# Kernel optimization log

Hardware: AMD Instinct MI355X
Metric: run time of the kernel (lower is better)

The kernel has to match this reference:

```python
import jax, jax.numpy as jnp
import numpy as np

TOP_K = 10
RANKING_WEIGHT = 0.3
UP_WEIGHT = 1.0
DOWN_WEIGHT = 0.5
NEG = 1e9  # finite stand-in for -inf so softmax/grads stay NaN-free


def setup_inputs() -> dict:
    key = jax.random.key(0)
    k1, k2, k3, k4 = jax.random.split(key, 4)
    B, N = 1024, 5000
    up_logits = jax.random.normal(k1, (B, N), jnp.float32)
    down_logits = jax.random.normal(k2, (B, N), jnp.float32)
    y_true = jax.random.normal(k3, (B, N), jnp.float32) * 0.05  # daily returns
    masks = jax.random.randint(k4, (B, N), 0, 2).astype(jnp.int32)
    return {"up_logits": up_logits, "down_logits": down_logits,
            "y_true": y_true, "masks": masks}


def _bce_with_logits(x, z):
    # softplus(x) - x*z  ==  -[z*log(sig(x)) + (1-z)*log(1-sig(x))]
    return jax.nn.softplus(x) - x * z


def reference(up_logits, down_logits, y_true, masks):
    maskb = masks > 0                                   # [B, N]
    maskf = maskb.astype(up_logits.dtype)
    num_valid = maskf.sum(-1)                           # [B]
    nv_safe = jnp.maximum(num_valid, 1.0)
    k = jnp.minimum(TOP_K, num_valid.astype(jnp.int32))  # [B] min(top_k, num)

    # Descending rank of y_true among valid entries (invalid pushed to bottom).
    y_desc = jnp.where(maskb, y_true, -NEG)
    rank_desc = jnp.argsort(jnp.argsort(-y_desc, axis=-1), axis=-1)  # [B, N]
    up_labels = (rank_desc < k[:, None]).astype(up_logits.dtype)

    # Ascending rank (biggest losers) for down path.
    y_asc = jnp.where(maskb, y_true, NEG)
    rank_asc = jnp.argsort(jnp.argsort(y_asc, axis=-1), axis=-1)
    down_labels = (rank_asc < k[:, None]).astype(down_logits.dtype)

    # Mean BCE over valid entries per row.
    up_loss = jnp.sum(_bce_with_logits(up_logits, up_labels) * maskf, -1) / nv_safe
    down_loss = jnp.sum(_bce_with_logits(down_logits, down_labels) * maskf, -1) / nv_safe

    # Listwise KL: softmax over valid entries; kl_div(log p, q, 'batchmean')
    # with 1D input of size num divides the sum by num.
    logp = jax.nn.log_softmax(jnp.where(maskb, up_logits, -NEG), axis=-1)
    logq = jax.nn.log_softmax(jnp.where(maskb, y_true, -NEG), axis=-1)
    q = jnp.exp(logq)
    kl = jnp.sum(jnp.where(maskb, q * (logq - logp), 0.0), -1) / nv_safe

    batch_loss = UP_WEIGHT * up_loss + DOWN_WEIGHT * down_loss + RANKING_WEIGHT * kl
    batch_loss = jnp.where(num_valid > 0, batch_loss, 0.0)  # skip empty rows
    return jnp.sum(batch_loss) / up_logits.shape[0]
```

## Files before the change

### kernel.cpp

```cpp
#include <hip/hip_runtime.h>
#include <math.h>

#define NCOLS 5000
#define NF4   1250
#define BLOCK 256
#define NWAVES (BLOCK / 64)
#define NITER 5
#define TOPKK 10
#define CAP 384

__device__ __forceinline__ unsigned mono_f32(float f) {
  unsigned u = __float_as_uint(f);
  return (u & 0x80000000u) ? ~u : (u | 0x80000000u);
}

__device__ __forceinline__ float wave_sum_f(float v) {
#pragma unroll
  for (int o = 1; o < 64; o <<= 1) v += __shfl_xor(v, o);
  return v;
}
__device__ __forceinline__ int wave_sum_i(int v) {
#pragma unroll
  for (int o = 1; o < 64; o <<= 1) v += __shfl_xor(v, o);
  return v;
}
__device__ __forceinline__ unsigned wave_max_u(unsigned v) {
#pragma unroll
  for (int o = 1; o < 64; o <<= 1) {
    unsigned w = __shfl_xor(v, o);
    v = w > v ? w : v;
  }
  return v;
}

extern "C" __global__ __launch_bounds__(BLOCK, 4)
void row_loss_kernel(const float* __restrict__ up, const float* __restrict__ down,
                     const float* __restrict__ yt, const int* __restrict__ masks,
                     float* __restrict__ out, float inv_nrows) {
  __shared__ float red_f[6][NWAVES];
  __shared__ int red_i[NWAVES];
  __shared__ unsigned t1w_t[NWAVES];
  __shared__ unsigned t1w_b[NWAVES];
  __shared__ unsigned keys_t[CAP];
  __shared__ int      col_t[CAP];
  __shared__ unsigned keys_b[CAP];
  __shared__ int      col_b[CAP];
  __shared__ int ct, cb;
  __shared__ float s_res[2];

  const int tid = threadIdx.x;
  const int lane = tid & 63;
  const int wv = tid >> 6;
  const int row = blockIdx.x;
  const long long b4 = (long long)row * NF4;
  const long long base = (long long)row * NCOLS;

  const float4* up4 = (const float4*)up + b4;
  const float4* dn4 = (const float4*)down + b4;
  const float4* yt4 = (const float4*)yt + b4;
  const int4*   mk4 = (const int4*)masks + b4;

  if (tid == 0) { ct = 0; cb = 0; }

  unsigned km[NITER][4];
  int nv_l = 0;
  float sq = 0.f, sp = 0.f, seyy = 0.f, seyu = 0.f;
  float pu0 = 1.f, pu1 = 1.f, pd0 = 1.f, pd1 = 1.f;
  unsigned tmax = 0u, tbmax = 0u;
#pragma unroll
  for (int j = 0; j < NITER; ++j) {
    const int f = j * BLOCK + tid;
    const int fc = f < NF4 ? f : NF4 - 1;
    const float4 y4 = yt4[fc];
    const float4 u4 = up4[fc];
    const float4 d4 = dn4[fc];
    const int4   m4 = mk4[fc];
    const bool inb = f < NF4;
    const float* yp = (const float*)&y4;
    const float* upp = (const float*)&u4;
    const float* dp = (const float*)&d4;
    const int* mp = (const int*)&m4;
#pragma unroll
    for (int c = 0; c < 4; ++c) {
      const bool valid = inb && (mp[c] > 0);
      const float y = valid ? yp[c] : -1000.f;
      const float u = valid ? upp[c] : -1000.f;
      const float d = valid ? dp[c] : -1000.f;
      const unsigned kd = valid ? mono_f32(y) : 0u;
      const unsigned kb = valid ? ~kd : 0u;
      km[j][c] = kd;
      tmax = kd > tmax ? kd : tmax;
      tbmax = kb > tbmax ? kb : tbmax;
      nv_l += valid ? 1 : 0;
      const float ey = __expf(y);
      const float eu = __expf(u);
      const float ed = __expf(d);
      sq += ey;
      seyy += ey * y;
      seyu += ey * u;
      sp += eu;
      if (j < 3) { pu0 *= 1.f + eu; pd0 *= 1.f + ed; }
      else       { pu1 *= 1.f + eu; pd1 *= 1.f + ed; }
    }
  }
  float aspu = __logf(pu0) + __logf(pu1);
  float aspd = __logf(pd0) + __logf(pd1);

  nv_l = wave_sum_i(nv_l);
  sq = wave_sum_f(sq);
  sp = wave_sum_f(sp);
  seyy = wave_sum_f(seyy);
  seyu = wave_sum_f(seyu);
  aspu = wave_sum_f(aspu);
  aspd = wave_sum_f(aspd);
  if (lane == 0) {
    red_i[wv] = nv_l;
    red_f[0][wv] = sq;  red_f[1][wv] = sp;
    red_f[2][wv] = seyy; red_f[3][wv] = seyu;
    red_f[4][wv] = aspu; red_f[5][wv] = aspd;
  }

  {
    unsigned v = tmax, t1 = 0u;
#pragma unroll 1
    for (int r = 0; r < TOPKK; ++r) {
      unsigned m = wave_max_u(v);
      if (v == m) v = 0u;
      t1 = m;
    }
    if (lane == 0) t1w_t[wv] = t1;
  }
  {
    unsigned v = tbmax, t1 = 0u;
#pragma unroll 1
    for (int r = 0; r < TOPKK; ++r) {
      unsigned m = wave_max_u(v);
      if (v == m) v = 0u;
      t1 = m;
    }
    if (lane == 0) t1w_b[wv] = t1;
  }
  __syncthreads();

  int nv = 0;
#pragma unroll
  for (int w = 0; w < NWAVES; ++w) nv += red_i[w];
  const int k = nv < TOPKK ? nv : TOPKK;

  unsigned t1 = 0u, t1b = 0u;
#pragma unroll
  for (int w = 0; w < NWAVES; ++w) {
    t1 = t1w_t[w] > t1 ? t1w_t[w] : t1;
    t1b = t1w_b[w] > t1b ? t1w_b[w] : t1b;
  }

#pragma unroll
  for (int j = 0; j < NITER; ++j) {
#pragma unroll
    for (int c = 0; c < 4; ++c) {
      const unsigned kd = km[j][c];
      if (kd != 0u) {
        const int col = ((j * BLOCK + tid) << 2) + c;
        if (kd >= t1) {
          int i = atomicAdd(&ct, 1);
          if (i < CAP) { keys_t[i] = kd; col_t[i] = col; }
        }
        const unsigned kb = ~kd;
        if (kb >= t1b) {
          int i = atomicAdd(&cb, 1);
          if (i < CAP) { keys_b[i] = kb; col_b[i] = col; }
        }
      }
    }
  }
  __syncthreads();

  if (wv == 0) {
    const int n = ct < CAP ? ct : CAP;
    unsigned kk[6];
#pragma unroll
    for (int i = 0; i < 6; ++i) {
      const int idx = i * 64 + lane;
      kk[i] = (idx < n) ? keys_t[idx] : 0u;
    }
    unsigned w0 = kk[0], w1 = kk[1], w2 = kk[2], w3 = kk[3], w4 = kk[4], w5 = kk[5];
    unsigned thr = 0xFFFFFFFFu;
#pragma unroll 1
    for (int r = 0; r < k; ++r) {
      unsigned l0 = w0 > w1 ? w0 : w1;
      unsigned l1 = w2 > w3 ? w2 : w3;
      unsigned l2 = w4 > w5 ? w4 : w5;
      l0 = l0 > l1 ? l0 : l1;
      unsigned m = wave_max_u(l0 > l2 ? l0 : l2);
      if (w0 == m) w0 = 0u;
      else if (w1 == m) w1 = 0u;
      else if (w2 == m) w2 = 0u;
      else if (w3 == m) w3 = 0u;
      else if (w4 == m) w4 = 0u;
      else if (w5 == m) w5 = 0u;
      thr = m;
    }
    float su = 0.f;
#pragma unroll
    for (int i = 0; i < 6; ++i) {
      const int idx = i * 64 + lane;
      if (kk[i] >= thr && kk[i] != 0u) su += up[base + col_t[idx]];
    }
    su = wave_sum_f(su);
    if (lane == 0) s_res[0] = su;
  } else if (wv == 1) {
    const int n = cb < CAP ? cb : CAP;
    unsigned kk[6];
#pragma unroll
    for (int i = 0; i < 6; ++i) {
      const int idx = i * 64 + lane;
      kk[i] = (idx < n) ? keys_b[idx] : 0u;
    }
    unsigned w0 = kk[0], w1 = kk[1], w2 = kk[2], w3 = kk[3], w4 = kk[4], w5 = kk[5];
    unsigned thr = 0xFFFFFFFFu;
#pragma unroll 1
    for (int r = 0; r < k; ++r) {
      unsigned l0 = w0 > w1 ? w0 : w1;
      unsigned l1 = w2 > w3 ? w2 : w3;
      unsigned l2 = w4 > w5 ? w4 : w5;
      l0 = l0 > l1 ? l0 : l1;
      unsigned m = wave_max_u(l0 > l2 ? l0 : l2);
      if (w0 == m) w0 = 0u;
      else if (w1 == m) w1 = 0u;
      else if (w2 == m) w2 = 0u;
      else if (w3 == m) w3 = 0u;
      else if (w4 == m) w4 = 0u;
      else if (w5 == m) w5 = 0u;
      thr = m;
    }
    float sd = 0.f;
#pragma unroll
    for (int i = 0; i < 6; ++i) {
      const int idx = i * 64 + lane;
      if (kk[i] >= thr && kk[i] != 0u) sd += down[base + col_b[idx]];
    }
    sd = wave_sum_f(sd);
    if (lane == 0) s_res[1] = sd;
  }
  __syncthreads();

  if (tid == 0 && nv > 0) {
    float SQ = 0.f, SP = 0.f, SYY = 0.f, SYU = 0.f, ASU = 0.f, ASD = 0.f;
#pragma unroll
    for (int w = 0; w < NWAVES; ++w) {
      SQ += red_f[0][w]; SP += red_f[1][w];
      SYY += red_f[2][w]; SYU += red_f[3][w];
      ASU += red_f[4][w]; ASD += red_f[5][w];
    }
    const float SU = s_res[0];
    const float SD = s_res[1];
    const float kl = (SYY - SYU) / SQ - __logf(SQ) + __logf(SP);
    const float up_loss = ASU - SU;
    const float dn_loss = ASD - SD;
    const float loss = (up_loss + 0.5f * dn_loss + 0.3f * kl) / (float)nv;
    atomicAdd(out, loss * inv_nrows);
  }
}

extern "C" void kernel_launch(void* const* d_in, const int* in_sizes, int n_in,
                              void* d_out, int out_size, void* d_ws, size_t ws_size,
                              hipStream_t stream) {
  const float* up_logits   = (const float*)d_in[0];
  const float* down_logits = (const float*)d_in[1];
  const float* y_true      = (const float*)d_in[2];
  const int*   masks       = (const int*)d_in[3];

  const int nrows = in_sizes[0] / NCOLS;

  hipMemsetAsync(d_out, 0, sizeof(float) * (size_t)out_size, stream);
  row_loss_kernel<<<nrows, BLOCK, 0, stream>>>(up_logits, down_logits, y_true,
                                               masks, (float*)d_out,
                                               1.0f / (float)nrows);
}
```

Measured before the change: 125.0 us.

## Split each row across two blocks and merge per-half top-k in finalize kernel

Each row is now processed by two 640-thread blocks, each handling half the columns with a single float4 per thread. Each block writes partial sums plus its local top-10 keys and values to workspace. A second kernel merges the two halves per row and reduces the loss. Candidate values are stored in shared memory directly, so the later global gathers of logits go away. The aim is more parallelism and latency hiding, at the cost of an extra kernel launch and a workspace round trip.

```diff
diff --git a/kernel.cpp b/kernel.cpp
--- a/kernel.cpp
+++ b/kernel.cpp
@@ -3,11 +3,13 @@
 
 #define NCOLS 5000
 #define NF4   1250
-#define BLOCK 256
-#define NWAVES (BLOCK / 64)
-#define NITER 5
+#define HALF_F4 625
+#define BLOCK_A 640
+#define NWAVES_A 10
 #define TOPKK 10
-#define CAP 384
+#define CAP 512
+#define WS_STRIDE 48
+#define BLOCK_B 256
 
 __device__ __forceinline__ unsigned mono_f32(float f) {
   unsigned u = __float_as_uint(f);
@@ -33,78 +35,71 @@
   return v;
 }
 
-extern "C" __global__ __launch_bounds__(BLOCK, 4)
-void row_loss_kernel(const float* __restrict__ up, const float* __restrict__ down,
-                     const float* __restrict__ yt, const int* __restrict__ masks,
-                     float* __restrict__ out, float inv_nrows) {
-  __shared__ float red_f[6][NWAVES];
-  __shared__ int red_i[NWAVES];
-  __shared__ unsigned t1w_t[NWAVES];
-  __shared__ unsigned t1w_b[NWAVES];
-  __shared__ unsigned keys_t[CAP];
-  __shared__ int      col_t[CAP];
-  __shared__ unsigned keys_b[CAP];
-  __shared__ int      col_b[CAP];
+extern "C" __global__ __launch_bounds__(BLOCK_A)
+void partial_kernel(const float* __restrict__ up, const float* __restrict__ down,
+                    const float* __restrict__ yt, const int* __restrict__ masks,
+                    float* __restrict__ ws) {
+  __shared__ float red_f[6][NWAVES_A];
+  __shared__ int red_i[NWAVES_A];
+  __shared__ unsigned t1w_t[NWAVES_A], t1w_b[NWAVES_A];
+  __shared__ unsigned skeys_t[CAP];
+  __shared__ float    svals_t[CAP];
+  __shared__ unsigned skeys_b[CAP];
+  __shared__ float    svals_b[CAP];
   __shared__ int ct, cb;
-  __shared__ float s_res[2];
 
   const int tid = threadIdx.x;
   const int lane = tid & 63;
   const int wv = tid >> 6;
-  const int row = blockIdx.x;
-  const long long b4 = (long long)row * NF4;
-  const long long base = (long long)row * NCOLS;
-
-  const float4* up4 = (const float4*)up + b4;
-  const float4* dn4 = (const float4*)down + b4;
-  const float4* yt4 = (const float4*)yt + b4;
-  const int4*   mk4 = (const int4*)masks + b4;
+  const int half = blockIdx.x & 1;
+  const int row = blockIdx.x >> 1;
+  const long long b4 = (long long)row * NF4 + half * HALF_F4;
 
   if (tid == 0) { ct = 0; cb = 0; }
 
-  unsigned km[NITER][4];
+  const bool inb = tid < HALF_F4;
+  const int fo = inb ? tid : HALF_F4 - 1;
+  const float4 y4 = ((const float4*)yt)[b4 + fo];
+  const float4 u4 = ((const float4*)up)[b4 + fo];
+  const float4 d4 = ((const float4*)down)[b4 + fo];
+  const int4   m4 = ((const int4*)masks)[b4 + fo];
+
+  unsigned km[4];
+  float uv[4], dv[4];
   int nv_l = 0;
   float sq = 0.f, sp = 0.f, seyy = 0.f, seyu = 0.f;
-  float pu0 = 1.f, pu1 = 1.f, pd0 = 1.f, pd1 = 1.f;
+  float pu = 1.f, pd = 1.f;
   unsigned tmax = 0u, tbmax = 0u;
-#pragma unroll
-  for (int j = 0; j < NITER; ++j) {
-    const int f = j * BLOCK + tid;
-    const int fc = f < NF4 ? f : NF4 - 1;
-    const float4 y4 = yt4[fc];
-    const float4 u4 = up4[fc];
-    const float4 d4 = dn4[fc];
-    const int4   m4 = mk4[fc];
-    const bool inb = f < NF4;
-    const float* yp = (const float*)&y4;
-    const float* upp = (const float*)&u4;
-    const float* dp = (const float*)&d4;
-    const int* mp = (const int*)&m4;
-#pragma unroll
-    for (int c = 0; c < 4; ++c) {
-      const bool valid = inb && (mp[c] > 0);
-      const float y = valid ? yp[c] : -1000.f;
-      const float u = valid ? upp[c] : -1000.f;
-      const float d = valid ? dp[c] : -1000.f;
-      const unsigned kd = valid ? mono_f32(y) : 0u;
-      const unsigned kb = valid ? ~kd : 0u;
-      km[j][c] = kd;
-      tmax = kd > tmax ? kd : tmax;
-      tbmax = kb > tbmax ? kb : tbmax;
-      nv_l += valid ? 1 : 0;
-      const float ey = __expf(y);
-      const float eu = __expf(u);
-      const float ed = __expf(d);
-      sq += ey;
-      seyy += ey * y;
-      seyu += ey * u;
-      sp += eu;
-      if (j < 3) { pu0 *= 1.f + eu; pd0 *= 1.f + ed; }
-      else       { pu1 *= 1.f + eu; pd1 *= 1.f + ed; }
-    }
-  }
-  float aspu = __logf(pu0) + __logf(pu1);
-  float aspd = __logf(pd0) + __logf(pd1);
+  const float* yp = (const float*)&y4;
+  const float* upp = (const float*)&u4;
+  const float* dp = (const float*)&d4;
+  const int* mp = (const int*)&m4;
+#pragma unroll
+  for (int c = 0; c < 4; ++c) {
+    const bool valid = inb && (mp[c] > 0);
+    const float y = valid ? yp[c] : -1000.f;
+    const float u = valid ? upp[c] : -1000.f;
+    const float d = valid ? dp[c] : -1000.f;
+    const unsigned kd = valid ? mono_f32(y) : 0u;
+    km[c] = kd;
+    uv[c] = u;
+    dv[c] = d;
+    const unsigned kb = valid ? ~kd : 0u;
+    tmax = kd > tmax ? kd : tmax;
+    tbmax = kb > tbmax ? kb : tbmax;
+    nv_l += valid ? 1 : 0;
+    const float ey = __expf(y);
+    const float eu = __expf(u);
+    const float ed = __expf(d);
+    sq += ey;
+    seyy += ey * y;
+    seyu += ey * u;
+    sp += eu;
+    pu *= 1.f + eu;
+    pd *= 1.f + ed;
+  }
+  float aspu = __logf(pu);
+  float aspd = __logf(pd);
 
   nv_l = wave_sum_i(nv_l);
   sq = wave_sum_f(sq);
@@ -142,124 +137,169 @@
   }
   __syncthreads();
 
-  int nv = 0;
-#pragma unroll
-  for (int w = 0; w < NWAVES; ++w) nv += red_i[w];
-  const int k = nv < TOPKK ? nv : TOPKK;
-
   unsigned t1 = 0u, t1b = 0u;
 #pragma unroll
-  for (int w = 0; w < NWAVES; ++w) {
+  for (int w = 0; w < NWAVES_A; ++w) {
     t1 = t1w_t[w] > t1 ? t1w_t[w] : t1;
     t1b = t1w_b[w] > t1b ? t1w_b[w] : t1b;
   }
 
 #pragma unroll
-  for (int j = 0; j < NITER; ++j) {
-#pragma unroll
-    for (int c = 0; c < 4; ++c) {
-      const unsigned kd = km[j][c];
-      if (kd != 0u) {
-        const int col = ((j * BLOCK + tid) << 2) + c;
-        if (kd >= t1) {
-          int i = atomicAdd(&ct, 1);
-          if (i < CAP) { keys_t[i] = kd; col_t[i] = col; }
-        }
-        const unsigned kb = ~kd;
-        if (kb >= t1b) {
-          int i = atomicAdd(&cb, 1);
-          if (i < CAP) { keys_b[i] = kb; col_b[i] = col; }
-        }
+  for (int c = 0; c < 4; ++c) {
+    const unsigned kd = km[c];
+    if (kd != 0u) {
+      if (kd >= t1) {
+        int i = atomicAdd(&ct, 1);
+        if (i < CAP) { skeys_t[i] = kd; svals_t[i] = uv[c]; }
+      }
+      const unsigned kb = ~kd;
+      if (kb >= t1b) {
+        int i = atomicAdd(&cb, 1);
+        if (i < CAP) { skeys_b[i] = kb; svals_b[i] = dv[c]; }
       }
     }
   }
   __syncthreads();
 
-  if (wv == 0) {
-    const int n = ct < CAP ? ct : CAP;
-    unsigned kk[6];
-#pragma unroll
-    for (int i = 0; i < 6; ++i) {
-      const int idx = i * 64 + lane;
-      kk[i] = (idx < n) ? keys_t[idx] : 0u;
-    }
-    unsigned w0 = kk[0], w1 = kk[1], w2 = kk[2], w3 = kk[3], w4 = kk[4], w5 = kk[5];
-    unsigned thr = 0xFFFFFFFFu;
-#pragma unroll 1
-    for (int r = 0; r < k; ++r) {
-      unsigned l0 = w0 > w1 ? w0 : w1;
-      unsigned l1 = w2 > w3 ? w2 : w3;
-      unsigned l2 = w4 > w5 ? w4 : w5;
-      l0 = l0 > l1 ? l0 : l1;
-      unsigned m = wave_max_u(l0 > l2 ? l0 : l2);
-      if (w0 == m) w0 = 0u;
-      else if (w1 == m) w1 = 0u;
-      else if (w2 == m) w2 = 0u;
-      else if (w3 == m) w3 = 0u;
-      else if (w4 == m) w4 = 0u;
-      else if (w5 == m) w5 = 0u;
-      thr = m;
-    }
-    float su = 0.f;
-#pragma unroll
-    for (int i = 0; i < 6; ++i) {
-      const int idx = i * 64 + lane;
-      if (kk[i] >= thr && kk[i] != 0u) su += up[base + col_t[idx]];
-    }
-    su = wave_sum_f(su);
-    if (lane == 0) s_res[0] = su;
-  } else if (wv == 1) {
-    const int n = cb < CAP ? cb : CAP;
-    unsigned kk[6];
-#pragma unroll
-    for (int i = 0; i < 6; ++i) {
-      const int idx = i * 64 + lane;
-      kk[i] = (idx < n) ? keys_b[idx] : 0u;
-    }
-    unsigned w0 = kk[0], w1 = kk[1], w2 = kk[2], w3 = kk[3], w4 = kk[4], w5 = kk[5];
-    unsigned thr = 0xFFFFFFFFu;
-#pragma unroll 1
-    for (int r = 0; r < k; ++r) {
-      unsigned l0 = w0 > w1 ? w0 : w1;
-      unsigned l1 = w2 > w3 ? w2 : w3;
-      unsigned l2 = w4 > w5 ? w4 : w5;
-      l0 = l0 > l1 ? l0 : l1;
-      unsigned m = wave_max_u(l0 > l2 ? l0 : l2);
-      if (w0 == m) w0 = 0u;
-      else if (w1 == m) w1 = 0u;
-      else if (w2 == m) w2 = 0u;
-      else if (w3 == m) w3 = 0u;
-      else if (w4 == m) w4 = 0u;
-      else if (w5 == m) w5 = 0u;
-      thr = m;
-    }
-    float sd = 0.f;
-#pragma unroll
-    for (int i = 0; i < 6; ++i) {
-      const int idx = i * 64 + lane;
-      if (kk[i] >= thr && kk[i] != 0u) sd += down[base + col_b[idx]];
-    }
-    sd = wave_sum_f(sd);
-    if (lane == 0) s_res[1] = sd;
-  }
-  __syncthreads();
-
-  if (tid == 0 && nv > 0) {
+  float* wsh = ws + (size_t)blockIdx.x * WS_STRIDE;
+
+  if (tid == 0) {
+    int nv = 0;
     float SQ = 0.f, SP = 0.f, SYY = 0.f, SYU = 0.f, ASU = 0.f, ASD = 0.f;
 #pragma unroll
-    for (int w = 0; w < NWAVES; ++w) {
+    for (int w = 0; w < NWAVES_A; ++w) {
+      nv += red_i[w];
       SQ += red_f[0][w]; SP += red_f[1][w];
       SYY += red_f[2][w]; SYU += red_f[3][w];
       ASU += red_f[4][w]; ASD += red_f[5][w];
     }
-    const float SU = s_res[0];
-    const float SD = s_res[1];
-    const float kl = (SYY - SYU) / SQ - __logf(SQ) + __logf(SP);
-    const float up_loss = ASU - SU;
-    const float dn_loss = ASD - SD;
-    const float loss = (up_loss + 0.5f * dn_loss + 0.3f * kl) / (float)nv;
-    atomicAdd(out, loss * inv_nrows);
-  }
+    wsh[0] = __uint_as_float((unsigned)nv);
+    wsh[1] = SQ; wsh[2] = SP; wsh[3] = SYY; wsh[4] = SYU;
+    wsh[5] = ASU; wsh[6] = ASD; wsh[7] = 0.f;
+  }
+
+  if (wv == 0) {
+    const int n = ct < CAP ? ct : CAP;
+    unsigned kk[8];
+#pragma unroll
+    for (int i = 0; i < 8; ++i) {
+      const int idx = i * 64 + lane;
+      kk[i] = (idx < n) ? skeys_t[idx] : 0u;
+    }
+#pragma unroll 1
+    for (int r = 0; r < TOPKK; ++r) {
+      unsigned lm = 0u;
+#pragma unroll
+      for (int i = 0; i < 8; ++i) lm = kk[i] > lm ? kk[i] : lm;
+      const unsigned m = wave_max_u(lm);
+      float vm = 0.f;
+      bool done = false;
+#pragma unroll
+      for (int i = 0; i < 8; ++i) {
+        if (!done && m != 0u && kk[i] == m) {
+          vm = svals_t[i * 64 + lane];
+          kk[i] = 0u;
+          done = true;
+        }
+      }
+      vm = wave_sum_f(vm);
+      if (lane == 0) {
+        wsh[8 + r] = __uint_as_float(m);
+        wsh[18 + r] = vm;
+      }
+    }
+  } else if (wv == 1) {
+    const int n = cb < CAP ? cb : CAP;
+    unsigned kk[8];
+#pragma unroll
+    for (int i = 0; i < 8; ++i) {
+      const int idx = i * 64 + lane;
+      kk[i] = (idx < n) ? skeys_b[idx] : 0u;
+    }
+#pragma unroll 1
+    for (int r = 0; r < TOPKK; ++r) {
+      unsigned lm = 0u;
+#pragma unroll
+      for (int i = 0; i < 8; ++i) lm = kk[i] > lm ? kk[i] : lm;
+      const unsigned m = wave_max_u(lm);
+      float vm = 0.f;
+      bool done = false;
+#pragma unroll
+      for (int i = 0; i < 8; ++i) {
+        if (!done && m != 0u && kk[i] == m) {
+          vm = svals_b[i * 64 + lane];
+          kk[i] = 0u;
+          done = true;
+        }
+      }
+      vm = wave_sum_f(vm);
+      if (lane == 0) {
+        wsh[28 + r] = __uint_as_float(m);
+        wsh[38 + r] = vm;
+      }
+    }
+  }
+}
+
+extern "C" __global__ __launch_bounds__(BLOCK_B)
+void finalize_kernel(const float* __restrict__ ws, float* __restrict__ out,
+                     float inv_nrows, int nrows) {
+  const int row = blockIdx.x * BLOCK_B + threadIdx.x;
+  float loss = 0.f;
+  if (row < nrows) {
+    const float* h0 = ws + (size_t)(2 * row) * WS_STRIDE;
+    const float* h1 = h0 + WS_STRIDE;
+    const int nv = (int)__float_as_uint(h0[0]) + (int)__float_as_uint(h1[0]);
+    if (nv > 0) {
+      const float SQ = h0[1] + h1[1];
+      const float SP = h0[2] + h1[2];
+      const float SYY = h0[3] + h1[3];
+      const float SYU = h0[4] + h1[4];
+      const float ASU = h0[5] + h1[5];
+      const float ASD = h0[6] + h1[6];
+      const int k = nv < TOPKK ? nv : TOPKK;
+
+      unsigned tk[20]; float tv[20];
+      unsigned bk[20]; float bv[20];
+#pragma unroll
+      for (int i = 0; i < TOPKK; ++i) {
+        tk[i] = __float_as_uint(h0[8 + i]);  tv[i] = h0[18 + i];
+        tk[10 + i] = __float_as_uint(h1[8 + i]); tv[10 + i] = h1[18 + i];
+        bk[i] = __float_as_uint(h0[28 + i]); bv[i] = h0[38 + i];
+        bk[10 + i] = __float_as_uint(h1[28 + i]); bv[10 + i] = h1[38 + i];
+      }
+
+      float SU = 0.f, SD = 0.f;
+#pragma unroll
+      for (int r = 0; r < TOPKK; ++r) {
+        if (r < k) {
+          unsigned bm = 0u;
+#pragma unroll
+          for (int i = 0; i < 20; ++i) bm = tk[i] > bm ? tk[i] : bm;
+          bool done = false;
+#pragma unroll
+          for (int i = 0; i < 20; ++i) {
+            if (!done && bm != 0u && tk[i] == bm) { SU += tv[i]; tk[i] = 0u; done = true; }
+          }
+          unsigned bm2 = 0u;
+#pragma unroll
+          for (int i = 0; i < 20; ++i) bm2 = bk[i] > bm2 ? bk[i] : bm2;
+          bool done2 = false;
+#pragma unroll
+          for (int i = 0; i < 20; ++i) {
+            if (!done2 && bm2 != 0u && bk[i] == bm2) { SD += bv[i]; bk[i] = 0u; done2 = true; }
+          }
+        }
+      }
+
+      const float kl = (SYY - SYU) / SQ - __logf(SQ) + __logf(SP);
+      const float up_loss = ASU - SU;
+      const float dn_loss = ASD - SD;
+      loss = (up_loss + 0.5f * dn_loss + 0.3f * kl) / (float)nv;
+    }
+  }
+  loss = wave_sum_f(loss * inv_nrows);
+  if ((threadIdx.x & 63) == 0) atomicAdd(out, loss);
 }
 
 extern "C" void kernel_launch(void* const* d_in, const int* in_sizes, int n_in,
@@ -273,7 +313,8 @@
   const int nrows = in_sizes[0] / NCOLS;
 
   hipMemsetAsync(d_out, 0, sizeof(float) * (size_t)out_size, stream);
-  row_loss_kernel<<<nrows, BLOCK, 0, stream>>>(up_logits, down_logits, y_true,
-                                               masks, (float*)d_out,
-                                               1.0f / (float)nrows);
-}
+  partial_kernel<<<nrows * 2, BLOCK_A, 0, stream>>>(up_logits, down_logits,
+                                                    y_true, masks, (float*)d_ws);
+  finalize_kernel<<<(nrows + BLOCK_B - 1) / BLOCK_B, BLOCK_B, 0, stream>>>(
+      (const float*)d_ws, (float*)d_out, 1.0f / (float)nrows, nrows);
+}
```

Measured after the change: 173.0 us. +38.3%, slower.
